# Kernel tuning notes

Hardware: AMD Instinct MI355X
Metric: run time of the kernel (lower is better)

The kernel has to match this reference:

```python
import jax, jax.numpy as jnp
import numpy as np

# NF4 codebook (bitsandbytes nf4 quant_type), 16 levels in [-1, 1]
NF4 = jnp.array([
    -1.0, -0.6961928009986877, -0.5250730514526367, -0.39491748809814453,
    -0.28444138169288635, -0.18477343022823334, -0.09105003625154495, 0.0,
    0.07958029955625534, 0.16093020141124725, 0.24611230194568634,
    0.33791524171829224, 0.44070982933044434, 0.5626170039176941,
    0.7229568362236023, 1.0], dtype=jnp.float32)
BLOCK = 64  # bitsandbytes default quant block size

TOKENS, HD, M = 8192, 4096, 11008


def dequant_nf4(codes, scales):
    # codes: [out, in] int in [0,16); scales: [out, in//BLOCK] per-block absmax
    out_f, in_f = codes.shape
    w = NF4[codes].reshape(out_f, in_f // BLOCK, BLOCK) * scales[:, :, None]
    return w.reshape(out_f, in_f)


def setup_inputs() -> dict:
    key = jax.random.key(0)
    k = jax.random.split(key, 7)
    return {
        "x": jax.random.normal(k[0], (TOKENS, HD), dtype=jnp.float32),
        "gate_codes": jax.random.randint(k[1], (M, HD), 0, 16, dtype=jnp.int32),
        "gate_scales": jax.random.uniform(k[2], (M, HD // BLOCK), dtype=jnp.float32) * 0.1,
        "up_codes": jax.random.randint(k[3], (M, HD), 0, 16, dtype=jnp.int32),
        "up_scales": jax.random.uniform(k[4], (M, HD // BLOCK), dtype=jnp.float32) * 0.1,
        "down_codes": jax.random.randint(k[5], (HD, M), 0, 16, dtype=jnp.int32),
        "down_scales": jax.random.uniform(k[6], (HD, M // BLOCK), dtype=jnp.float32) * 0.1,
    }


def reference(x, gate_codes, gate_scales, up_codes, up_scales, down_codes, down_scales):
    Wg = dequant_nf4(gate_codes, gate_scales)   # [m, hd]
    Wu = dequant_nf4(up_codes, up_scales)       # [m, hd]
    Wd = dequant_nf4(down_codes, down_scales)   # [hd, m]
    g = jnp.einsum('td,md->tm', x, Wg)          # gate_proj(x)
    u = jnp.einsum('td,md->tm', x, Wu)          # up_proj(x)
    h = jax.nn.silu(g) * u                      # SwiGLU
    return jnp.einsum('tm,dm->td', h, Wd)       # down_proj
```

## Files before the change

kernel.cpp:

```cpp
#include <hip/hip_runtime.h>
#include <hip/hip_bf16.h>

typedef _Float16 half8 __attribute__((ext_vector_type(8)));
typedef float floatx4 __attribute__((ext_vector_type(4)));

__device__ __constant__ float NF4_TAB[16] = {
    -1.0f, -0.6961928009986877f, -0.5250730514526367f, -0.39491748809814453f,
    -0.28444138169288635f, -0.18477343022823334f, -0.09105003625154495f, 0.0f,
    0.07958029955625534f, 0.16093020141124725f, 0.24611230194568634f,
    0.33791524171829224f, 0.44070982933044434f, 0.5626170039176941f,
    0.7229568362236023f, 1.0f};

typedef __attribute__((address_space(3))) void lds_t;
typedef __attribute__((address_space(1))) void gbl_t;

__device__ __forceinline__ void gload16(const void* g, void* l) {
  __builtin_amdgcn_global_load_lds((gbl_t*)g, (lds_t*)l, 16, 0, 0);
}

__global__ void cvt_f32_to_f16(const float* __restrict__ in,
                               _Float16* __restrict__ out, int total8) {
  int stride = gridDim.x * blockDim.x;
  for (int i = blockIdx.x * blockDim.x + threadIdx.x; i < total8; i += stride) {
    long e = (long)i * 8;
    const float4* ip = reinterpret_cast<const float4*>(in + e);
    float4 a = ip[0], b = ip[1];
    half8 o;
    o[0] = (_Float16)a.x; o[1] = (_Float16)a.y;
    o[2] = (_Float16)a.z; o[3] = (_Float16)a.w;
    o[4] = (_Float16)b.x; o[5] = (_Float16)b.y;
    o[6] = (_Float16)b.z; o[7] = (_Float16)b.w;
    *reinterpret_cast<half8*>(out + e) = o;
  }
}

__global__ void dequant_nf4(const int* __restrict__ codes,
                            const float* __restrict__ scales,
                            _Float16* __restrict__ out,
                            int total8, int C, int CB) {
  __shared__ float lut[16];
  if (threadIdx.x < 16) lut[threadIdx.x] = NF4_TAB[threadIdx.x];
  __syncthreads();
  int stride = gridDim.x * blockDim.x;
  for (int i = blockIdx.x * blockDim.x + threadIdx.x; i < total8; i += stride) {
    long e = (long)i * 8;
    int row = (int)(e / C);
    int col = (int)(e - (long)row * C);
    float sc = scales[row * CB + (col >> 6)];
    const int4* cp = reinterpret_cast<const int4*>(codes + e);
    int4 c0 = cp[0];
    int4 c1 = cp[1];
    half8 o;
    o[0] = (_Float16)(lut[c0.x & 15] * sc);
    o[1] = (_Float16)(lut[c0.y & 15] * sc);
    o[2] = (_Float16)(lut[c0.z & 15] * sc);
    o[3] = (_Float16)(lut[c0.w & 15] * sc);
    o[4] = (_Float16)(lut[c1.x & 15] * sc);
    o[5] = (_Float16)(lut[c1.y & 15] * sc);
    o[6] = (_Float16)(lut[c1.z & 15] * sc);
    o[7] = (_Float16)(lut[c1.w & 15] * sc);
    *reinterpret_cast<half8*>(out + e) = o;
  }
}

template <int K, int N, int EPI>
__global__ __launch_bounds__(512, 2) void gemm256(
    const _Float16* __restrict__ A,
    const _Float16* __restrict__ B,
    _Float16* __restrict__ GH,
    float* __restrict__ OUT) {
  constexpr int NT = K / 64;
  constexpr int NBC = N / 256;
  constexpr int NWG = (8192 / 256) * NBC;
  __shared__ __align__(16) _Float16 lds[2 * 32768];

  const int t = threadIdx.x;
  const int lane = t & 63;
  const int wave = t >> 6;
  const int wm = wave >> 2;
  const int wn = wave & 3;

  int bid = blockIdx.x;
  bid = (bid & 7) * (NWG >> 3) + (bid >> 3);
  const int bm = bid / NBC, bn = bid % NBC;

  const int lc = (t & 3) ^ ((t >> 3) & 3);
  const _Float16* gA = A + ((long)bm * 256 + (t >> 2)) * K + lc * 8;
  const _Float16* gB = B + ((long)bn * 256 + (t >> 2)) * K + lc * 8;
  const long rstep = (long)128 * K;
  const int dst = t * 8;

  const int rA = wm * 128 + (lane & 15);
  const int rB = wn * 64 + (lane & 15);
  const int ckA = ((lane >> 4) ^ ((rA >> 1) & 3)) * 8;
  const int ckB = ((lane >> 4) ^ ((rB >> 1) & 3)) * 8;
  const int offA = rA * 32 + ckA;
  const int offB = 16384 + rB * 32 + ckB;

#define STAGE_SLOT(gp, slab, koff, dbuf)                                   \
  gload16((gp) + (koff), lds + (dbuf) * 32768 + (slab) + dst);             \
  gload16((gp) + (koff) + rstep, lds + (dbuf) * 32768 + (slab) + dst + 4096);

  STAGE_SLOT(gA, 0, 0, 0);
  STAGE_SLOT(gB, 16384, 0, 0);
  STAGE_SLOT(gA, 8192, 32, 0);
  STAGE_SLOT(gB, 24576, 32, 0);
  gA += 64; gB += 64;
  asm volatile("s_waitcnt vmcnt(4)" ::: "memory");
  __builtin_amdgcn_s_barrier();
  __builtin_amdgcn_sched_barrier(0);

  floatx4 acc[8][4] = {};

  for (int kt = 0; kt < NT; ++kt) {
    const int cb = kt & 1;
    const int sbuf = cb ^ 1;
    const _Float16* lb = lds + cb * 32768;
    const bool st = (kt + 1 < NT);
    const bool last = (kt == NT - 1);

    half8 a[8], b[2];

#pragma unroll
    for (int i = 0; i < 8; ++i)
      a[i] = *reinterpret_cast<const half8*>(&lb[offA + i * 512]);
    b[0] = *reinterpret_cast<const half8*>(&lb[offB]);
    b[1] = *reinterpret_cast<const half8*>(&lb[offB + 512]);
    if (st) { STAGE_SLOT(gA, 0, 0, sbuf); }
    __builtin_amdgcn_s_barrier();
    asm volatile("s_waitcnt lgkmcnt(0)" ::: "memory");
    __builtin_amdgcn_sched_barrier(0);
    __builtin_amdgcn_s_setprio(1);
#pragma unroll
    for (int i = 0; i < 8; ++i) {
      acc[i][0] = __builtin_amdgcn_mfma_f32_16x16x32_f16(a[i], b[0], acc[i][0], 0, 0, 0);
      acc[i][1] = __builtin_amdgcn_mfma_f32_16x16x32_f16(a[i], b[1], acc[i][1], 0, 0, 0);
    }
    __builtin_amdgcn_s_setprio(0);
    __builtin_amdgcn_s_barrier();
    __builtin_amdgcn_sched_barrier(0);

    b[0] = *reinterpret_cast<const half8*>(&lb[offB + 2 * 512]);
    b[1] = *reinterpret_cast<const half8*>(&lb[offB + 3 * 512]);
    if (st) { STAGE_SLOT(gB, 16384, 0, sbuf); }
    if (last) { asm volatile("s_waitcnt vmcnt(0)" ::: "memory"); }
    else      { asm volatile("s_waitcnt vmcnt(4)" ::: "memory"); }
    __builtin_amdgcn_s_barrier();
    asm volatile("s_waitcnt lgkmcnt(0)" ::: "memory");
    __builtin_amdgcn_sched_barrier(0);
    __builtin_amdgcn_s_setprio(1);
#pragma unroll
    for (int i = 0; i < 8; ++i) {
      acc[i][2] = __builtin_amdgcn_mfma_f32_16x16x32_f16(a[i], b[0], acc[i][2], 0, 0, 0);
      acc[i][3] = __builtin_amdgcn_mfma_f32_16x16x32_f16(a[i], b[1], acc[i][3], 0, 0, 0);
    }
    __builtin_amdgcn_s_setprio(0);
    __builtin_amdgcn_s_barrier();
    __builtin_amdgcn_sched_barrier(0);

#pragma unroll
    for (int i = 0; i < 8; ++i)
      a[i] = *reinterpret_cast<const half8*>(&lb[8192 + offA + i * 512]);
    b[0] = *reinterpret_cast<const half8*>(&lb[8192 + offB]);
    b[1] = *reinterpret_cast<const half8*>(&lb[8192 + offB + 512]);
    if (st) { STAGE_SLOT(gA, 8192, 32, sbuf); }
    __builtin_amdgcn_s_barrier();
    asm volatile("s_waitcnt lgkmcnt(0)" ::: "memory");
    __builtin_amdgcn_sched_barrier(0);
    __builtin_amdgcn_s_setprio(1);
#pragma unroll
    for (int i = 0; i < 8; ++i) {
      acc[i][0] = __builtin_amdgcn_mfma_f32_16x16x32_f16(a[i], b[0], acc[i][0], 0, 0, 0);
      acc[i][1] = __builtin_amdgcn_mfma_f32_16x16x32_f16(a[i], b[1], acc[i][1], 0, 0, 0);
    }
    __builtin_amdgcn_s_setprio(0);
    __builtin_amdgcn_s_barrier();
    __builtin_amdgcn_sched_barrier(0);

    b[0] = *reinterpret_cast<const half8*>(&lb[8192 + offB + 2 * 512]);
    b[1] = *reinterpret_cast<const half8*>(&lb[8192 + offB + 3 * 512]);
    if (st) { STAGE_SLOT(gB, 24576, 32, sbuf); gA += 64; gB += 64; }
    if (!last) { asm volatile("s_waitcnt vmcnt(4)" ::: "memory"); }
    __builtin_amdgcn_s_barrier();
    asm volatile("s_waitcnt lgkmcnt(0)" ::: "memory");
    __builtin_amdgcn_sched_barrier(0);
    __builtin_amdgcn_s_setprio(1);
#pragma unroll
    for (int i = 0; i < 8; ++i) {
      acc[i][2] = __builtin_amdgcn_mfma_f32_16x16x32_f16(a[i], b[0], acc[i][2], 0, 0, 0);
      acc[i][3] = __builtin_amdgcn_mfma_f32_16x16x32_f16(a[i], b[1], acc[i][3], 0, 0, 0);
    }
    __builtin_amdgcn_s_setprio(0);
    __builtin_amdgcn_s_barrier();
    __builtin_amdgcn_sched_barrier(0);
  }
#undef STAGE_SLOT

  const int r0 = bm * 256 + wm * 128 + (lane >> 4) * 4;
  const int c0 = bn * 256 + wn * 64 + (lane & 15);
#pragma unroll
  for (int i = 0; i < 8; ++i) {
#pragma unroll
    for (int j = 0; j < 4; ++j) {
#pragma unroll
      for (int ii = 0; ii < 4; ++ii) {
        const long idx = (long)(r0 + i * 16 + ii) * N + (c0 + j * 16);
        if (EPI == 0) {
          GH[idx] = (_Float16)acc[i][j][ii];
        } else if (EPI == 1) {
          float u = acc[i][j][ii];
          float g = (float)GH[idx];
          GH[idx] = (_Float16)(g / (1.0f + __expf(-g)) * u);
        } else {
          OUT[idx] = acc[i][j][ii];
        }
      }
    }
  }
}

extern "C" void kernel_launch(void* const* d_in, const int* in_sizes, int n_in,
                              void* d_out, int out_size, void* d_ws, size_t ws_size,
                              hipStream_t stream) {
  const float* x           = (const float*)d_in[0];
  const int*   gate_codes  = (const int*)d_in[1];
  const float* gate_scales = (const float*)d_in[2];
  const int*   up_codes    = (const int*)d_in[3];
  const float* up_scales   = (const float*)d_in[4];
  const int*   down_codes  = (const int*)d_in[5];
  const float* down_scales = (const float*)d_in[6];
  float* out = (float*)d_out;

  const long T = 8192, HD = 4096, M = 11008;

  char* ws = (char*)d_ws;
  _Float16* x16 = (_Float16*)ws;
  _Float16* W   = (_Float16*)(ws + T * HD * 2);
  _Float16* gh  = (_Float16*)(ws + T * HD * 2 + M * HD * 2);

  cvt_f32_to_f16<<<2048, 256, 0, stream>>>(x, x16, (int)(T * HD / 8));

  dequant_nf4<<<2048, 256, 0, stream>>>(gate_codes, gate_scales, W,
                                        (int)(M * HD / 8), (int)HD, (int)(HD / 64));
  gemm256<4096, 11008, 0><<<(8192 / 256) * (11008 / 256), 512, 0, stream>>>(
      x16, W, gh, nullptr);

  dequant_nf4<<<2048, 256, 0, stream>>>(up_codes, up_scales, W,
                                        (int)(M * HD / 8), (int)HD, (int)(HD / 64));
  gemm256<4096, 11008, 1><<<(8192 / 256) * (11008 / 256), 512, 0, stream>>>(
      x16, W, gh, nullptr);

  dequant_nf4<<<2048, 256, 0, stream>>>(down_codes, down_scales, W,
                                        (int)(HD * M / 8), (int)M, (int)(M / 64));
  gemm256<11008, 4096, 2><<<(8192 / 256) * (4096 / 256), 512, 0, stream>>>(
      gh, W, nullptr, out);
}
```

Baseline: 2.303 ms.

## Restructure GEMM main loop into quadrant-ordered MFMA with B prefetched two stages ahead

```diff
diff --git a/kernel.cpp b/kernel.cpp
--- a/kernel.cpp
+++ b/kernel.cpp
@@ -71,7 +71,9 @@
     float* __restrict__ OUT) {
   constexpr int NT = K / 64;
   constexpr int NBC = N / 256;
-  constexpr int NWG = (8192 / 256) * NBC;
+  constexpr int NFULL = NBC / 8;
+  constexpr int TAILW = NBC - 8 * NFULL;
+  constexpr int FULLB = NFULL * 256;
   __shared__ __align__(16) _Float16 lds[2 * 32768];
 
   const int t = threadIdx.x;
@@ -80,15 +82,32 @@
   const int wm = wave >> 2;
   const int wn = wave & 3;
 
-  int bid = blockIdx.x;
-  bid = (bid & 7) * (NWG >> 3) + (bid >> 3);
-  const int bm = bid / NBC, bn = bid % NBC;
+  int bm, bn;
+  {
+    const int bid = blockIdx.x;
+    if (bid < FULLB) {
+      const int g = bid >> 8;
+      const int r = bid & 255;
+      bm = r >> 3;
+      bn = g * 8 + (r & 7);
+    } else if (TAILW > 0) {
+      const int r = bid - FULLB;
+      bm = r / (TAILW > 0 ? TAILW : 1);
+      bn = NFULL * 8 + r % (TAILW > 0 ? TAILW : 1);
+    } else {
+      bm = 0; bn = 0;
+    }
+  }
 
   const int lc = (t & 3) ^ ((t >> 3) & 3);
   const _Float16* gA = A + ((long)bm * 256 + (t >> 2)) * K + lc * 8;
   const _Float16* gB = B + ((long)bn * 256 + (t >> 2)) * K + lc * 8;
   const long rstep = (long)128 * K;
   const int dst = t * 8;
+
+#define STAGE_SLOT(gp, slab, koff, dbuf)                                   \
+  gload16((gp) + (koff), lds + (dbuf) * 32768 + (slab) + dst);             \
+  gload16((gp) + (koff) + rstep, lds + (dbuf) * 32768 + (slab) + dst + 4096);
 
   const int rA = wm * 128 + (lane & 15);
   const int rB = wn * 64 + (lane & 15);
@@ -97,100 +116,117 @@
   const int offA = rA * 32 + ckA;
   const int offB = 16384 + rB * 32 + ckB;
 
-#define STAGE_SLOT(gp, slab, koff, dbuf)                                   \
-  gload16((gp) + (koff), lds + (dbuf) * 32768 + (slab) + dst);             \
-  gload16((gp) + (koff) + rstep, lds + (dbuf) * 32768 + (slab) + dst + 4096);
-
-  STAGE_SLOT(gA, 0, 0, 0);
-  STAGE_SLOT(gB, 16384, 0, 0);
-  STAGE_SLOT(gA, 8192, 32, 0);
-  STAGE_SLOT(gB, 24576, 32, 0);
-  gA += 64; gB += 64;
+  STAGE_SLOT(gB, 16384, 0, 0);  STAGE_SLOT(gB, 24576, 32, 0);
+  STAGE_SLOT(gA, 0, 0, 0);      STAGE_SLOT(gA, 8192, 32, 0);
+  STAGE_SLOT(gB, 16384, 64, 1); STAGE_SLOT(gB, 24576, 96, 1);
+  gA += 64;
+  gB += 128;
   asm volatile("s_waitcnt vmcnt(4)" ::: "memory");
   __builtin_amdgcn_s_barrier();
   __builtin_amdgcn_sched_barrier(0);
 
   floatx4 acc[8][4] = {};
+  half8 b0[4], b1[4], a[8];
+
+#pragma unroll
+  for (int jj = 0; jj < 2; ++jj)
+#pragma unroll
+    for (int kk = 0; kk < 2; ++kk)
+      b0[jj * 2 + kk] = *reinterpret_cast<const half8*>(&lds[offB + jj * 512 + kk * 8192]);
 
   for (int kt = 0; kt < NT; ++kt) {
     const int cb = kt & 1;
-    const int sbuf = cb ^ 1;
+    const int sb = cb ^ 1;
     const _Float16* lb = lds + cb * 32768;
-    const bool st = (kt + 1 < NT);
-    const bool last = (kt == NT - 1);
-
-    half8 a[8], b[2];
-
-#pragma unroll
-    for (int i = 0; i < 8; ++i)
-      a[i] = *reinterpret_cast<const half8*>(&lb[offA + i * 512]);
-    b[0] = *reinterpret_cast<const half8*>(&lb[offB]);
-    b[1] = *reinterpret_cast<const half8*>(&lb[offB + 512]);
-    if (st) { STAGE_SLOT(gA, 0, 0, sbuf); }
+    const bool stA = (kt + 1 < NT);
+    const bool stB = (kt + 2 < NT);
+
+#pragma unroll
+    for (int rr = 0; rr < 4; ++rr)
+#pragma unroll
+      for (int kk = 0; kk < 2; ++kk)
+        a[rr * 2 + kk] = *reinterpret_cast<const half8*>(&lb[offA + rr * 512 + kk * 8192]);
+    if (stA) { STAGE_SLOT(gA, 0, 0, sb); STAGE_SLOT(gA, 8192, 32, sb); gA += 64; }
     __builtin_amdgcn_s_barrier();
     asm volatile("s_waitcnt lgkmcnt(0)" ::: "memory");
     __builtin_amdgcn_sched_barrier(0);
     __builtin_amdgcn_s_setprio(1);
 #pragma unroll
-    for (int i = 0; i < 8; ++i) {
-      acc[i][0] = __builtin_amdgcn_mfma_f32_16x16x32_f16(a[i], b[0], acc[i][0], 0, 0, 0);
-      acc[i][1] = __builtin_amdgcn_mfma_f32_16x16x32_f16(a[i], b[1], acc[i][1], 0, 0, 0);
-    }
-    __builtin_amdgcn_s_setprio(0);
-    __builtin_amdgcn_s_barrier();
-    __builtin_amdgcn_sched_barrier(0);
-
-    b[0] = *reinterpret_cast<const half8*>(&lb[offB + 2 * 512]);
-    b[1] = *reinterpret_cast<const half8*>(&lb[offB + 3 * 512]);
-    if (st) { STAGE_SLOT(gB, 16384, 0, sbuf); }
-    if (last) { asm volatile("s_waitcnt vmcnt(0)" ::: "memory"); }
-    else      { asm volatile("s_waitcnt vmcnt(4)" ::: "memory"); }
+    for (int rr = 0; rr < 4; ++rr)
+#pragma unroll
+      for (int kk = 0; kk < 2; ++kk)
+#pragma unroll
+        for (int jj = 0; jj < 2; ++jj)
+          acc[rr][jj] = __builtin_amdgcn_mfma_f32_16x16x32_f16(a[rr * 2 + kk], b0[jj * 2 + kk], acc[rr][jj], 0, 0, 0);
+    __builtin_amdgcn_s_setprio(0);
+    __builtin_amdgcn_s_barrier();
+    __builtin_amdgcn_sched_barrier(0);
+
+#pragma unroll
+    for (int jj = 0; jj < 2; ++jj)
+#pragma unroll
+      for (int kk = 0; kk < 2; ++kk)
+        b1[jj * 2 + kk] = *reinterpret_cast<const half8*>(&lb[offB + 1024 + jj * 512 + kk * 8192]);
     __builtin_amdgcn_s_barrier();
     asm volatile("s_waitcnt lgkmcnt(0)" ::: "memory");
     __builtin_amdgcn_sched_barrier(0);
     __builtin_amdgcn_s_setprio(1);
 #pragma unroll
-    for (int i = 0; i < 8; ++i) {
-      acc[i][2] = __builtin_amdgcn_mfma_f32_16x16x32_f16(a[i], b[0], acc[i][2], 0, 0, 0);
-      acc[i][3] = __builtin_amdgcn_mfma_f32_16x16x32_f16(a[i], b[1], acc[i][3], 0, 0, 0);
-    }
-    __builtin_amdgcn_s_setprio(0);
-    __builtin_amdgcn_s_barrier();
-    __builtin_amdgcn_sched_barrier(0);
-
-#pragma unroll
-    for (int i = 0; i < 8; ++i)
-      a[i] = *reinterpret_cast<const half8*>(&lb[8192 + offA + i * 512]);
-    b[0] = *reinterpret_cast<const half8*>(&lb[8192 + offB]);
-    b[1] = *reinterpret_cast<const half8*>(&lb[8192 + offB + 512]);
-    if (st) { STAGE_SLOT(gA, 8192, 32, sbuf); }
+    for (int rr = 0; rr < 4; ++rr)
+#pragma unroll
+      for (int kk = 0; kk < 2; ++kk)
+#pragma unroll
+        for (int jj = 0; jj < 2; ++jj)
+          acc[rr][2 + jj] = __builtin_amdgcn_mfma_f32_16x16x32_f16(a[rr * 2 + kk], b1[jj * 2 + kk], acc[rr][2 + jj], 0, 0, 0);
+    __builtin_amdgcn_s_setprio(0);
+    __builtin_amdgcn_s_barrier();
+    __builtin_amdgcn_sched_barrier(0);
+
+#pragma unroll
+    for (int rr = 0; rr < 4; ++rr)
+#pragma unroll
+      for (int kk = 0; kk < 2; ++kk)
+        a[rr * 2 + kk] = *reinterpret_cast<const half8*>(&lb[offA + 2048 + rr * 512 + kk * 8192]);
     __builtin_amdgcn_s_barrier();
     asm volatile("s_waitcnt lgkmcnt(0)" ::: "memory");
     __builtin_amdgcn_sched_barrier(0);
     __builtin_amdgcn_s_setprio(1);
 #pragma unroll
-    for (int i = 0; i < 8; ++i) {
-      acc[i][0] = __builtin_amdgcn_mfma_f32_16x16x32_f16(a[i], b[0], acc[i][0], 0, 0, 0);
-      acc[i][1] = __builtin_amdgcn_mfma_f32_16x16x32_f16(a[i], b[1], acc[i][1], 0, 0, 0);
-    }
-    __builtin_amdgcn_s_setprio(0);
-    __builtin_amdgcn_s_barrier();
-    __builtin_amdgcn_sched_barrier(0);
-
-    b[0] = *reinterpret_cast<const half8*>(&lb[8192 + offB + 2 * 512]);
-    b[1] = *reinterpret_cast<const half8*>(&lb[8192 + offB + 3 * 512]);
-    if (st) { STAGE_SLOT(gB, 24576, 32, sbuf); gA += 64; gB += 64; }
-    if (!last) { asm volatile("s_waitcnt vmcnt(4)" ::: "memory"); }
-    __builtin_amdgcn_s_barrier();
-    asm volatile("s_waitcnt lgkmcnt(0)" ::: "memory");
-    __builtin_amdgcn_sched_barrier(0);
-    __builtin_amdgcn_s_setprio(1);
-#pragma unroll
-    for (int i = 0; i < 8; ++i) {
-      acc[i][2] = __builtin_amdgcn_mfma_f32_16x16x32_f16(a[i], b[0], acc[i][2], 0, 0, 0);
-      acc[i][3] = __builtin_amdgcn_mfma_f32_16x16x32_f16(a[i], b[1], acc[i][3], 0, 0, 0);
-    }
-    __builtin_amdgcn_s_setprio(0);
+    for (int rr = 0; rr < 4; ++rr)
+#pragma unroll
+      for (int kk = 0; kk < 2; ++kk)
+#pragma unroll
+        for (int jj = 0; jj < 2; ++jj)
+          acc[4 + rr][jj] = __builtin_amdgcn_mfma_f32_16x16x32_f16(a[rr * 2 + kk], b0[jj * 2 + kk], acc[4 + rr][jj], 0, 0, 0);
+    __builtin_amdgcn_s_setprio(0);
+    if (stA) { asm volatile("s_waitcnt vmcnt(4)" ::: "memory"); }
+    __builtin_amdgcn_s_barrier();
+    __builtin_amdgcn_sched_barrier(0);
+
+    if (stA) {
+      const _Float16* nb = lds + sb * 32768;
+#pragma unroll
+      for (int jj = 0; jj < 2; ++jj)
+#pragma unroll
+        for (int kk = 0; kk < 2; ++kk)
+          b0[jj * 2 + kk] = *reinterpret_cast<const half8*>(&nb[offB + jj * 512 + kk * 8192]);
+    }
+    if (stB) { STAGE_SLOT(gB, 16384, 0, cb); STAGE_SLOT(gB, 24576, 32, cb); gB += 64; }
+    __builtin_amdgcn_s_barrier();
+    __builtin_amdgcn_sched_barrier(0);
+    __builtin_amdgcn_s_setprio(1);
+#pragma unroll
+    for (int rr = 0; rr < 4; ++rr)
+#pragma unroll
+      for (int kk = 0; kk < 2; ++kk)
+#pragma unroll
+        for (int jj = 0; jj < 2; ++jj)
+          acc[4 + rr][2 + jj] = __builtin_amdgcn_mfma_f32_16x16x32_f16(a[rr * 2 + kk], b1[jj * 2 + kk], acc[4 + rr][2 + jj], 0, 0, 0);
+    __builtin_amdgcn_s_setprio(0);
+    if (stA) {
+      if (stB) { asm volatile("s_waitcnt vmcnt(4)" ::: "memory"); }
+      else     { asm volatile("s_waitcnt vmcnt(0)" ::: "memory"); }
+    }
     __builtin_amdgcn_s_barrier();
     __builtin_amdgcn_sched_barrier(0);
   }
```

After: 2.483 ms. +7.8%, slower.
